# Kernel tuning notes

Hardware: AMD Instinct MI355X
Metric: run time of the kernel (lower is better)

The kernel has to match this reference:

```python
import jax, jax.numpy as jnp
import numpy as np

N, E, F_IN, D, H, G, T = 30000, 480000, 128, 32, 4, 128, 10
HD = H * D
NEG_SLOPE = 0.2


def _lin(key, fan_out, fan_in, scale=0.05):
    k1, k2 = jax.random.split(key)
    return (jax.random.normal(k1, (fan_out, fan_in), jnp.float32) * scale,
            jax.random.normal(k2, (fan_out,), jnp.float32) * scale)


def setup_inputs() -> dict:
    key = jax.random.key(0)
    ks = jax.random.split(key, 24)
    x = jax.random.normal(ks[0], (N, F_IN), jnp.float32)
    edge_index = jax.random.randint(ks[1], (2, E), 0, N, jnp.int64)
    batch = jnp.sort(jax.random.randint(ks[2], (N,), 0, G, jnp.int64))
    inp = {"x": x, "edge_index": edge_index, "batch": batch}
    # conv 0 (in=F_IN) and conv 1 (in=D); each followed by Linear(HD -> D)
    for i, fin in enumerate([F_IN, D]):
        base = 3 + i * 8
        Wl, bl = _lin(ks[base + 0], HD, fin)
        Wr, br = _lin(ks[base + 1], HD, fin)
        att = jax.random.normal(ks[base + 2], (H, D), jnp.float32) * 0.05
        bias = jnp.zeros((HD,), jnp.float32)
        lw, lb = _lin(ks[base + 3], D, HD)
        inp.update({f"Wl{i}": Wl, f"bl{i}": bl, f"Wr{i}": Wr, f"br{i}": br,
                    f"att{i}": att, f"cb{i}": bias, f"lw{i}": lw, f"lb{i}": lb})
    inp["fc1_W"], inp["fc1_b"] = _lin(ks[20], D, D)
    inp["fc2_W"], inp["fc2_b"] = _lin(ks[21], T, D)
    return inp


def _gatv2_conv(x, src, dst, Wl, bl, Wr, br, att, bias):
    # PyG GATv2Conv, concat=True, add_self_loops already applied to src/dst,
    # aggr='mean', eval mode (no dropout).
    n = x.shape[0]
    xl = (x @ Wl.T + bl).reshape(n, H, D)
    xr = (x @ Wr.T + br).reshape(n, H, D)
    e = jax.nn.leaky_relu(xl[src] + xr[dst], NEG_SLOPE)          # [E', H, D]
    alpha = jnp.einsum('ehd,hd->eh', e, att)                      # [E', H]
    amax = jax.ops.segment_max(alpha, dst, num_segments=n)        # [n, H]
    ex = jnp.exp(alpha - amax[dst])
    denom = jax.ops.segment_sum(ex, dst, num_segments=n)
    a = ex / denom[dst]                                           # softmax per target
    msg = xl[src] * a[:, :, None]                                 # [E', H, D]
    s = jax.ops.segment_sum(msg, dst, num_segments=n)
    cnt = jax.ops.segment_sum(jnp.ones((src.shape[0],), jnp.float32), dst, num_segments=n)
    out = s / cnt[:, None, None]                                  # mean aggregation
    return out.reshape(n, HD) + bias


def reference(x, edge_index, batch,
              Wl0, bl0, Wr0, br0, att0, cb0, lw0, lb0,
              Wl1, bl1, Wr1, br1, att1, cb1, lw1, lb1,
              fc1_W, fc1_b, fc2_W, fc2_b):
    loop = jnp.arange(N, dtype=edge_index.dtype)
    src = jnp.concatenate([edge_index[0], loop])  # add self loops
    dst = jnp.concatenate([edge_index[1], loop])
    convs = [(Wl0, bl0, Wr0, br0, att0, cb0, lw0, lb0),
             (Wl1, bl1, Wr1, br1, att1, cb1, lw1, lb1)]
    h = x
    for (Wl, bl, Wr, br, att, cb, lw, lb) in convs:
        h = _gatv2_conv(h, src, dst, Wl, bl, Wr, br, att, cb)
        h = h @ lw.T + lb  # heads>1: Linear(H*D -> D)
    g = jax.ops.segment_max(h, batch, num_segments=G)  # global max pool
    g = jax.nn.relu(g @ fc1_W.T + fc1_b)
    return g @ fc2_W.T + fc2_b
```

## Files before the change

### kernel.cpp

```cpp
#include <hip/hip_runtime.h>
#include <hip/hip_bf16.h>

#define NEG_SLOPE 0.2f
#define GGRP 128
#define TOUT 10

__global__ void init_kernel(int* __restrict__ deg, float* __restrict__ gpool,
                            int n, int gsize) {
    int i = blockIdx.x * blockDim.x + threadIdx.x;
    if (i < n) deg[i] = 0;
    if (i < gsize) gpool[i] = -__builtin_inff();
}

__global__ void degree_kernel(const int* __restrict__ dst, int* __restrict__ deg, int E) {
    int i = blockIdx.x * blockDim.x + threadIdx.x;
    int base = i * 4;
    if (base + 3 < E) {
        int4 d = *(const int4*)(dst + base);
        atomicAdd(&deg[d.x], 1); atomicAdd(&deg[d.y], 1);
        atomicAdd(&deg[d.z], 1); atomicAdd(&deg[d.w], 1);
    } else {
        for (int k = base; k < E; ++k) atomicAdd(&deg[dst[k]], 1);
    }
}

__global__ __launch_bounds__(256)
void scanA_kernel(const int* __restrict__ deg, int* __restrict__ rowptr,
                  int* __restrict__ bsum, int n) {
    __shared__ int wsum[4];
    int tid = threadIdx.x, lane = tid & 63, wid = tid >> 6;
    int idx = blockIdx.x * 256 + tid;
    int v = (idx < n) ? deg[idx] : 0;
    int x = v;
    #pragma unroll
    for (int off = 1; off < 64; off <<= 1) {
        int t = __shfl_up(x, off, 64);
        if (lane >= off) x += t;
    }
    if (lane == 63) wsum[wid] = x;
    __syncthreads();
    if (tid == 0) {
        int s = 0;
        #pragma unroll
        for (int i = 0; i < 4; ++i) { int t = wsum[i]; wsum[i] = s; s += t; }
        bsum[blockIdx.x] = s;
    }
    __syncthreads();
    int excl = x - v + wsum[wid];
    if (idx < n) rowptr[idx] = excl;
}

__global__ void scanB_kernel(const int* __restrict__ bsum, int* __restrict__ boff,
                             int* __restrict__ rowptr, int n, int nb) {
    int lane = threadIdx.x;
    int v0 = (lane < nb) ? bsum[lane] : 0;
    int v1 = (64 + lane < nb) ? bsum[64 + lane] : 0;
    int s0 = v0, s1 = v1;
    #pragma unroll
    for (int off = 1; off < 64; off <<= 1) {
        int t0 = __shfl_up(s0, off, 64);
        int t1 = __shfl_up(s1, off, 64);
        if (lane >= off) { s0 += t0; s1 += t1; }
    }
    int tot0 = __shfl(s0, 63, 64);
    s1 += tot0;
    boff[lane] = s0 - v0;
    boff[64 + lane] = s1 - v1;
    if (lane == 63) rowptr[n] = s1;
}

__global__ void scanC_kernel(int* __restrict__ rowptr, int* __restrict__ cursor,
                             const int* __restrict__ boff, int n) {
    int idx = blockIdx.x * blockDim.x + threadIdx.x;
    if (idx < n) {
        int r = rowptr[idx] + boff[idx >> 8];
        rowptr[idx] = r;
        cursor[idx] = r;
    }
}

__global__ void scatter_kernel(const int* __restrict__ src, const int* __restrict__ dst,
                               int* __restrict__ cursor, int* __restrict__ csr, int E) {
    int i = blockIdx.x * blockDim.x + threadIdx.x;
    int base = i * 4;
    if (base + 3 < E) {
        int4 s = *(const int4*)(src + base);
        int4 d = *(const int4*)(dst + base);
        csr[atomicAdd(&cursor[d.x], 1)] = s.x;
        csr[atomicAdd(&cursor[d.y], 1)] = s.y;
        csr[atomicAdd(&cursor[d.z], 1)] = s.z;
        csr[atomicAdd(&cursor[d.w], 1)] = s.w;
    } else {
        for (int k = base; k < E; ++k)
            csr[atomicAdd(&cursor[dst[k]], 1)] = src[k];
    }
}

template <int FIN>
__global__ __launch_bounds__(256, 2)
void gemm_tile_kernel(const float* __restrict__ X,
                      const float* __restrict__ Wl, const float* __restrict__ bl,
                      const float* __restrict__ Wr, const float* __restrict__ br,
                      float* __restrict__ xl, float* __restrict__ xr,
                      int n, int nRowBlk) {
    constexpr int BK = 32, BM = 128, LDA = BM + 4;
    constexpr int NCHUNK = FIN / BK;
    __shared__ float Xs[BK][LDA];
    __shared__ float Ws[BK][LDA];
    int tid = threadIdx.x;
    int rowBlk = blockIdx.x;
    int colBlk = 0;
    if (rowBlk >= nRowBlk) { rowBlk -= nRowBlk; colBlk = 1; }
    const float* __restrict__ Wb = colBlk ? Wr : Wl;
    const float* __restrict__ bb = colBlk ? br : bl;
    float* __restrict__ ob = colBlk ? xr : xl;
    int row0 = rowBlk * BM;

    int sr  = tid >> 3;
    int skq = (tid & 7) * 4;

    float4 xpre[4], wpre[4];

    auto load_pre = [&](int c) {
        int k0 = c * BK;
        #pragma unroll
        for (int i = 0; i < 4; ++i) {
            int r = sr + i * 32;
            int gr = row0 + r;
            float4 v = {0.f, 0.f, 0.f, 0.f};
            if (gr < n) v = *(const float4*)&X[(size_t)gr * FIN + k0 + skq];
            xpre[i] = v;
            wpre[i] = *(const float4*)&Wb[(size_t)r * FIN + k0 + skq];
        }
    };
    auto store_pre = [&]() {
        #pragma unroll
        for (int i = 0; i < 4; ++i) {
            int r = sr + i * 32;
            Xs[skq + 0][r] = xpre[i].x; Xs[skq + 1][r] = xpre[i].y;
            Xs[skq + 2][r] = xpre[i].z; Xs[skq + 3][r] = xpre[i].w;
            Ws[skq + 0][r] = wpre[i].x; Ws[skq + 1][r] = wpre[i].y;
            Ws[skq + 2][r] = wpre[i].z; Ws[skq + 3][r] = wpre[i].w;
        }
    };

    load_pre(0);
    store_pre();
    __syncthreads();

    int tx = tid & 15;
    int ty = tid >> 4;
    float acc[8][8];
    #pragma unroll
    for (int i = 0; i < 8; ++i)
        #pragma unroll
        for (int j = 0; j < 8; ++j) acc[i][j] = 0.f;

    #pragma unroll
    for (int c = 0; c < NCHUNK; ++c) {
        if (c + 1 < NCHUNK) load_pre(c + 1);
        #pragma unroll 8
        for (int k = 0; k < BK; ++k) {
            float4 a0 = *(const float4*)&Xs[k][ty * 8];
            float4 a1 = *(const float4*)&Xs[k][ty * 8 + 4];
            float4 b0 = *(const float4*)&Ws[k][tx * 8];
            float4 b1 = *(const float4*)&Ws[k][tx * 8 + 4];
            float av[8] = {a0.x, a0.y, a0.z, a0.w, a1.x, a1.y, a1.z, a1.w};
            float bv[8] = {b0.x, b0.y, b0.z, b0.w, b1.x, b1.y, b1.z, b1.w};
            #pragma unroll
            for (int i = 0; i < 8; ++i)
                #pragma unroll
                for (int j = 0; j < 8; ++j)
                    acc[i][j] = fmaf(av[i], bv[j], acc[i][j]);
        }
        if (c + 1 < NCHUNK) {
            __syncthreads();
            store_pre();
            __syncthreads();
        }
    }

    float bias[8];
    #pragma unroll
    for (int j = 0; j < 8; ++j) bias[j] = bb[tx * 8 + j];
    #pragma unroll
    for (int i = 0; i < 8; ++i) {
        int gr = row0 + ty * 8 + i;
        if (gr < n) {
            float4 o0, o1;
            o0.x = acc[i][0] + bias[0]; o0.y = acc[i][1] + bias[1];
            o0.z = acc[i][2] + bias[2]; o0.w = acc[i][3] + bias[3];
            o1.x = acc[i][4] + bias[4]; o1.y = acc[i][5] + bias[5];
            o1.z = acc[i][6] + bias[6]; o1.w = acc[i][7] + bias[7];
            *(float4*)&ob[(size_t)gr * 128 + tx * 8]     = o0;
            *(float4*)&ob[(size_t)gr * 128 + tx * 8 + 4] = o1;
        }
    }
}

__global__ __launch_bounds__(256)
void gat_fused_kernel(const float* __restrict__ xl, const float* __restrict__ xr,
                      const float* __restrict__ att, const float* __restrict__ cb,
                      const float* __restrict__ lw, const float* __restrict__ lb,
                      const int* __restrict__ rowptr, const int* __restrict__ csr,
                      float* __restrict__ out , int n) {
    __shared__ float lws[32][132];
    __shared__ float oslot[4][128];
    int tid = threadIdx.x;
    #pragma unroll
    for (int i = 0; i < 16; ++i) {
        int idx = tid + i * 256;
        lws[idx >> 7][idx & 127] = lw[idx];
    }
    __syncthreads();

    int wid = tid >> 6, lane = tid & 63;
    int q4  = lane >> 4;
    int l16 = lane & 15;
    int f8  = l16 * 8;
    int half = lane >> 5;
    int l32  = lane & 31;

    const float4 atA = *(const float4*)(att + f8);
    const float4 atB = *(const float4*)(att + f8 + 4);
    const float4 cbA = *(const float4*)(cb + f8);
    const float4 cbB = *(const float4*)(cb + f8 + 4);
    float lbv = lb[l32];

    int ndBase = blockIdx.x * 16 + wid * 4;

    for (int j = 0; j < 4; ++j) {
        int nd = ndBase + j;
        if (nd >= n) break;

        const float4 xrA  = *(const float4*)(xr + (size_t)nd * 128 + f8);
        const float4 xrB  = *(const float4*)(xr + (size_t)nd * 128 + f8 + 4);
        const float4 xlsA = *(const float4*)(xl + (size_t)nd * 128 + f8);
        const float4 xlsB = *(const float4*)(xl + (size_t)nd * 128 + f8 + 4);

        int start = rowptr[nd], end = rowptr[nd + 1];

        float den;
        float accA[4] = {0.f, 0.f, 0.f, 0.f};
        float accB[4] = {0.f, 0.f, 0.f, 0.f};

        {
            float e0 = xlsA.x + xrA.x; e0 = e0 > 0.f ? e0 : NEG_SLOPE * e0;
            float e1 = xlsA.y + xrA.y; e1 = e1 > 0.f ? e1 : NEG_SLOPE * e1;
            float e2 = xlsA.z + xrA.z; e2 = e2 > 0.f ? e2 : NEG_SLOPE * e2;
            float e3 = xlsA.w + xrA.w; e3 = e3 > 0.f ? e3 : NEG_SLOPE * e3;
            float e4 = xlsB.x + xrB.x; e4 = e4 > 0.f ? e4 : NEG_SLOPE * e4;
            float e5 = xlsB.y + xrB.y; e5 = e5 > 0.f ? e5 : NEG_SLOPE * e5;
            float e6 = xlsB.z + xrB.z; e6 = e6 > 0.f ? e6 : NEG_SLOPE * e6;
            float e7 = xlsB.w + xrB.w; e7 = e7 > 0.f ? e7 : NEG_SLOPE * e7;
            float q = e0 * atA.x + e1 * atA.y + e2 * atA.z + e3 * atA.w
                    + e4 * atB.x + e5 * atB.y + e6 * atB.z + e7 * atB.w;
            q += __shfl_xor(q, 1); q += __shfl_xor(q, 2);
            float a = __expf(q);
            if (q4 == 0) {
                den = a;
                accA[0] = a * xlsA.x; accA[1] = a * xlsA.y;
                accA[2] = a * xlsA.z; accA[3] = a * xlsA.w;
                accB[0] = a * xlsB.x; accB[1] = a * xlsB.y;
                accB[2] = a * xlsB.z; accB[3] = a * xlsB.w;
            } else {
                den = 0.f;
            }
        }

        int i = start + q4;
        int sA = (i < end) ? csr[i] : 0;
        int sB = (i + 4 < end) ? csr[i + 4] : 0;
        float4 pre0 = {0.f, 0.f, 0.f, 0.f}, pre1 = pre0;
        if (i < end) {
            pre0 = *(const float4*)(xl + (size_t)sA * 128 + f8);
            pre1 = *(const float4*)(xl + (size_t)sA * 128 + f8 + 4);
        }
        for (; i < end; i += 4) {
            float4 x0 = pre0, x1 = pre1;
            sA = sB;
            if (i + 8 < end) sB = csr[i + 8];
            if (i + 4 < end) {
                pre0 = *(const float4*)(xl + (size_t)sA * 128 + f8);
                pre1 = *(const float4*)(xl + (size_t)sA * 128 + f8 + 4);
            }
            float e0 = x0.x + xrA.x; e0 = e0 > 0.f ? e0 : NEG_SLOPE * e0;
            float e1 = x0.y + xrA.y; e1 = e1 > 0.f ? e1 : NEG_SLOPE * e1;
            float e2 = x0.z + xrA.z; e2 = e2 > 0.f ? e2 : NEG_SLOPE * e2;
            float e3 = x0.w + xrA.w; e3 = e3 > 0.f ? e3 : NEG_SLOPE * e3;
            float e4 = x1.x + xrB.x; e4 = e4 > 0.f ? e4 : NEG_SLOPE * e4;
            float e5 = x1.y + xrB.y; e5 = e5 > 0.f ? e5 : NEG_SLOPE * e5;
            float e6 = x1.z + xrB.z; e6 = e6 > 0.f ? e6 : NEG_SLOPE * e6;
            float e7 = x1.w + xrB.w; e7 = e7 > 0.f ? e7 : NEG_SLOPE * e7;
            float q = e0 * atA.x + e1 * atA.y + e2 * atA.z + e3 * atA.w
                    + e4 * atB.x + e5 * atB.y + e6 * atB.z + e7 * atB.w;
            q += __shfl_xor(q, 1); q += __shfl_xor(q, 2);
            float a = __expf(q);
            den += a;
            accA[0] = fmaf(a, x0.x, accA[0]); accA[1] = fmaf(a, x0.y, accA[1]);
            accA[2] = fmaf(a, x0.z, accA[2]); accA[3] = fmaf(a, x0.w, accA[3]);
            accB[0] = fmaf(a, x1.x, accB[0]); accB[1] = fmaf(a, x1.y, accB[1]);
            accB[2] = fmaf(a, x1.z, accB[2]); accB[3] = fmaf(a, x1.w, accB[3]);
        }

        #pragma unroll
        for (int t = 0; t < 4; ++t) {
            accA[t] += __shfl_xor(accA[t], 16); accA[t] += __shfl_xor(accA[t], 32);
            accB[t] += __shfl_xor(accB[t], 16); accB[t] += __shfl_xor(accB[t], 32);
        }
        den += __shfl_xor(den, 16); den += __shfl_xor(den, 32);

        float inv = 1.0f / (den * (float)(end - start + 1));
        if (q4 == 0) {
            float4 oA, oB;
            oA.x = fmaf(accA[0], inv, cbA.x); oA.y = fmaf(accA[1], inv, cbA.y);
            oA.z = fmaf(accA[2], inv, cbA.z); oA.w = fmaf(accA[3], inv, cbA.w);
            oB.x = fmaf(accB[0], inv, cbB.x); oB.y = fmaf(accB[1], inv, cbB.y);
            oB.z = fmaf(accB[2], inv, cbB.z); oB.w = fmaf(accB[3], inv, cbB.w);
            *(float4*)&oslot[wid][f8]     = oA;
            *(float4*)&oslot[wid][f8 + 4] = oB;
        }
        asm volatile("s_waitcnt lgkmcnt(0)" ::: "memory");

        float y = 0.f;
        int kbase = half * 64;
        #pragma unroll
        for (int k = 0; k < 64; k += 4) {
            float4 lv = *(const float4*)&lws[l32][kbase + k];
            float4 ov = *(const float4*)&oslot[wid][kbase + k];
            y = fmaf(lv.x, ov.x, y);
            y = fmaf(lv.y, ov.y, y);
            y = fmaf(lv.z, ov.z, y);
            y = fmaf(lv.w, ov.w, y);
        }
        y += __shfl_xor(y, 32);
        if (half == 0) out[(size_t)nd * 32 + l32] = y + lbv;
    }
}

__device__ __forceinline__ void atomicMaxFloat(float* addr, float val) {
    if (val >= 0.f) atomicMax((int*)addr, __float_as_int(val));
    else atomicMin((unsigned int*)addr, (unsigned int)__float_as_int(val));
}

__global__ void pool_kernel(const float* __restrict__ H, const int* __restrict__ batch,
                            float* __restrict__ g, int n) {
    int tid = threadIdx.x;
    int dim = tid & 31;
    int sub = tid >> 5;
    int nodeStart = blockIdx.x * 128 + sub * 16;
    float m = -__builtin_inff();
    int cur = -1;
    for (int j = 0; j < 16; ++j) {
        int nd = nodeStart + j;
        if (nd >= n) break;
        int b = batch[nd];
        if (b != cur) {
            if (cur >= 0) atomicMaxFloat(&g[cur * 32 + dim], m);
            cur = b; m = -__builtin_inff();
        }
        m = fmaxf(m, H[nd * 32 + dim]);
    }
    if (cur >= 0) atomicMaxFloat(&g[cur * 32 + dim], m);
}

__global__ __launch_bounds__(256)
void fc_kernel(const float* __restrict__ g,
               const float* __restrict__ fc1W, const float* __restrict__ fc1b,
               const float* __restrict__ fc2W, const float* __restrict__ fc2b,
               float* __restrict__ out) {
    __shared__ float g1[GGRP * 32];
    int tid = threadIdx.x;
    for (int idx = tid; idx < GGRP * 32; idx += 256) {
        int r = idx >> 5, c = idx & 31;
        float acc = fc1b[c];
        #pragma unroll
        for (int k = 0; k < 32; ++k) acc = fmaf(g[r * 32 + k], fc1W[c * 32 + k], acc);
        g1[idx] = acc > 0.f ? acc : 0.f;
    }
    __syncthreads();
    for (int idx = tid; idx < GGRP * TOUT; idx += 256) {
        int r = idx / TOUT, c = idx - r * TOUT;
        float acc = fc2b[c];
        #pragma unroll
        for (int k = 0; k < 32; ++k) acc = fmaf(g1[r * 32 + k], fc2W[c * 32 + k], acc);
        out[idx] = acc;
    }
}

extern "C" void kernel_launch(void* const* d_in, const int* in_sizes, int n_in,
                              void* d_out, int out_size, void* d_ws, size_t ws_size,
                              hipStream_t stream) {
    const float* x     = (const float*)d_in[0];
    const int*   ei    = (const int*)d_in[1];
    const int*   batch = (const int*)d_in[2];
    const float* Wl0 = (const float*)d_in[3];
    const float* bl0 = (const float*)d_in[4];
    const float* Wr0 = (const float*)d_in[5];
    const float* br0 = (const float*)d_in[6];
    const float* at0 = (const float*)d_in[7];
    const float* cb0 = (const float*)d_in[8];
    const float* lw0 = (const float*)d_in[9];
    const float* lb0 = (const float*)d_in[10];
    const float* Wl1 = (const float*)d_in[11];
    const float* bl1 = (const float*)d_in[12];
    const float* Wr1 = (const float*)d_in[13];
    const float* br1 = (const float*)d_in[14];
    const float* at1 = (const float*)d_in[15];
    const float* cb1 = (const float*)d_in[16];
    const float* lw1 = (const float*)d_in[17];
    const float* lb1 = (const float*)d_in[18];
    const float* fc1W = (const float*)d_in[19];
    const float* fc1b = (const float*)d_in[20];
    const float* fc2W = (const float*)d_in[21];
    const float* fc2b = (const float*)d_in[22];

    const int n = in_sizes[0] / 128;
    const int E = in_sizes[1] / 2;
    const int* src = ei;
    const int* dst = ei + E;
    const int nblkScan = (n + 255) / 256;
    const int nRowBlk = (n + 127) / 128;
    const int E4 = (E + 3) / 4;

    size_t off = 0;
    auto alloc = [&](size_t bytes) {
        void* p = (char*)d_ws + off;
        off += (bytes + 255) & ~(size_t)255;
        return p;
    };
    float* xl    = (float*)alloc((size_t)n * 128 * 4);
    float* xr    = (float*)alloc((size_t)n * 128 * 4);
    float* hbuf  = (float*)alloc((size_t)n * 32 * 4);
    int* deg     = (int*)alloc((size_t)n * 4);
    int* rowptr  = (int*)alloc((size_t)(n + 1) * 4);
    int* cursor  = (int*)alloc((size_t)n * 4);
    int* csr     = (int*)alloc((size_t)E * 4);
    int* bsum    = (int*)alloc(128 * 4);
    int* boff    = (int*)alloc(128 * 4);
    float* gpool = (float*)alloc((size_t)GGRP * 32 * 4);

    init_kernel<<<(n + 255) / 256, 256, 0, stream>>>(deg, gpool, n, GGRP * 32);
    degree_kernel<<<(E4 + 255) / 256, 256, 0, stream>>>(dst, deg, E);
    scanA_kernel<<<nblkScan, 256, 0, stream>>>(deg, rowptr, bsum, n);
    scanB_kernel<<<1, 64, 0, stream>>>(bsum, boff, rowptr, n, nblkScan);
    scanC_kernel<<<nblkScan, 256, 0, stream>>>(rowptr, cursor, boff, n);
    scatter_kernel<<<(E4 + 255) / 256, 256, 0, stream>>>(src, dst, cursor, csr, E);

    gemm_tile_kernel<128><<<2 * nRowBlk, 256, 0, stream>>>(x, Wl0, bl0, Wr0, br0,
                                                           xl, xr, n, nRowBlk);
    gat_fused_kernel<<<(n + 15) / 16, 256, 0, stream>>>(xl, xr, at0, cb0, lw0, lb0,
                                                        rowptr, csr, hbuf, n);
    gemm_tile_kernel<32><<<2 * nRowBlk, 256, 0, stream>>>(hbuf, Wl1, bl1, Wr1, br1,
                                                          xl, xr, n, nRowBlk);
    gat_fused_kernel<<<(n + 15) / 16, 256, 0, stream>>>(xl, xr, at1, cb1, lw1, lb1,
                                                        rowptr, csr, hbuf, n);

    pool_kernel<<<(n + 127) / 128, 256, 0, stream>>>(hbuf, batch, gpool, n);
    fc_kernel<<<1, 256, 0, stream>>>(gpool, fc1W, fc1b, fc2W, fc2b, (float*)d_out);
}
```

Measured before the change: 315.0 us.

## Store byte offsets in CSR, drop gather bounds checks, one node per wave

The scatter now stores source indices pre-shifted into byte offsets, and the CSR gets a zero-padded tail, so the GAT gather loop can prefetch without bounds checks or index multiplies. The GAT kernel maps one destination node per wavefront (4 per block) instead of looping over 4 nodes per wave, giving more blocks and parallelism at the cost of reloading lw into shared memory 4x more often. The separate scanB kernel is folded into scanC, where each block reduces the block sums itself, which removes one launch. Using 32-bit byte offsets limits the node count to about 4M.

New measurement: 308.0 us. -2.2%, faster.

```diff
diff --git a/kernel.cpp b/kernel.cpp
--- a/kernel.cpp
+++ b/kernel.cpp
@@ -6,10 +6,11 @@
 #define TOUT 10
 
 __global__ void init_kernel(int* __restrict__ deg, float* __restrict__ gpool,
-                            int n, int gsize) {
+                            int* __restrict__ csr_pad, int n, int gsize) {
     int i = blockIdx.x * blockDim.x + threadIdx.x;
     if (i < n) deg[i] = 0;
     if (i < gsize) gpool[i] = -__builtin_inff();
+    if (i < 64) csr_pad[i] = 0;
 }
 
 __global__ void degree_kernel(const int* __restrict__ dst, int* __restrict__ deg, int E) {
@@ -50,30 +51,33 @@
     if (idx < n) rowptr[idx] = excl;
 }
 
-__global__ void scanB_kernel(const int* __restrict__ bsum, int* __restrict__ boff,
-                             int* __restrict__ rowptr, int n, int nb) {
-    int lane = threadIdx.x;
-    int v0 = (lane < nb) ? bsum[lane] : 0;
-    int v1 = (64 + lane < nb) ? bsum[64 + lane] : 0;
-    int s0 = v0, s1 = v1;
-    #pragma unroll
-    for (int off = 1; off < 64; off <<= 1) {
-        int t0 = __shfl_up(s0, off, 64);
-        int t1 = __shfl_up(s1, off, 64);
-        if (lane >= off) { s0 += t0; s1 += t1; }
-    }
-    int tot0 = __shfl(s0, 63, 64);
-    s1 += tot0;
-    boff[lane] = s0 - v0;
-    boff[64 + lane] = s1 - v1;
-    if (lane == 63) rowptr[n] = s1;
-}
-
-__global__ void scanC_kernel(int* __restrict__ rowptr, int* __restrict__ cursor,
-                             const int* __restrict__ boff, int n) {
-    int idx = blockIdx.x * blockDim.x + threadIdx.x;
+__global__ __launch_bounds__(256)
+void scanC_kernel(int* __restrict__ rowptr, int* __restrict__ cursor,
+                  const int* __restrict__ bsum, int n, int nb) {
+    __shared__ int soff_sh;
+    int tid = threadIdx.x;
+    int bx = blockIdx.x;
+    if (tid < 64) {
+        int lane = tid;
+        int v = 0;
+        if (lane < nb && lane < bx) v = bsum[lane];
+        if (lane + 64 < nb && lane + 64 < bx) v += bsum[lane + 64];
+        #pragma unroll
+        for (int off = 32; off >= 1; off >>= 1) v += __shfl_xor(v, off, 64);
+        if (lane == 0) soff_sh = v;
+        if (bx == 0) {
+            int t = 0;
+            if (lane < nb) t = bsum[lane];
+            if (lane + 64 < nb) t += bsum[lane + 64];
+            #pragma unroll
+            for (int off = 32; off >= 1; off >>= 1) t += __shfl_xor(t, off, 64);
+            if (lane == 0) rowptr[n] = t;
+        }
+    }
+    __syncthreads();
+    int idx = bx * 256 + tid;
     if (idx < n) {
-        int r = rowptr[idx] + boff[idx >> 8];
+        int r = rowptr[idx] + soff_sh;
         rowptr[idx] = r;
         cursor[idx] = r;
     }
@@ -86,13 +90,13 @@
     if (base + 3 < E) {
         int4 s = *(const int4*)(src + base);
         int4 d = *(const int4*)(dst + base);
-        csr[atomicAdd(&cursor[d.x], 1)] = s.x;
-        csr[atomicAdd(&cursor[d.y], 1)] = s.y;
-        csr[atomicAdd(&cursor[d.z], 1)] = s.z;
-        csr[atomicAdd(&cursor[d.w], 1)] = s.w;
+        csr[atomicAdd(&cursor[d.x], 1)] = s.x << 9;
+        csr[atomicAdd(&cursor[d.y], 1)] = s.y << 9;
+        csr[atomicAdd(&cursor[d.z], 1)] = s.z << 9;
+        csr[atomicAdd(&cursor[d.w], 1)] = s.w << 9;
     } else {
         for (int k = base; k < E; ++k)
-            csr[atomicAdd(&cursor[dst[k]], 1)] = src[k];
+            csr[atomicAdd(&cursor[dst[k]], 1)] = src[k] << 9;
     }
 }
 
@@ -202,7 +206,7 @@
 void gat_fused_kernel(const float* __restrict__ xl, const float* __restrict__ xr,
                       const float* __restrict__ att, const float* __restrict__ cb,
                       const float* __restrict__ lw, const float* __restrict__ lb,
-                      const int* __restrict__ rowptr, const int* __restrict__ csr,
+                      const int* __restrict__ rowptr, const int* __restrict__ csrb,
                       float* __restrict__ out , int n) {
     __shared__ float lws[32][132];
     __shared__ float oslot[4][128];
@@ -215,127 +219,121 @@
     __syncthreads();
 
     int wid = tid >> 6, lane = tid & 63;
+    int nd = blockIdx.x * 4 + wid;
+    if (nd >= n) return;
     int q4  = lane >> 4;
     int l16 = lane & 15;
-    int f8  = l16 * 8;
+    int fb  = l16 * 32;
+
+    const char* __restrict__ xlb = (const char*)xl;
+    const char* __restrict__ xrb = (const char*)xr;
+    int selfoff = nd << 9;
+
+    const float4 xrA  = *(const float4*)(xrb + selfoff + fb);
+    const float4 xrB  = *(const float4*)(xrb + selfoff + fb + 16);
+    const float4 atA  = *(const float4*)((const char*)att + fb);
+    const float4 atB  = *(const float4*)((const char*)att + fb + 16);
+    const float4 xlsA = *(const float4*)(xlb + selfoff + fb);
+    const float4 xlsB = *(const float4*)(xlb + selfoff + fb + 16);
+
+    int start = rowptr[nd], end = rowptr[nd + 1];
+    float cnt = (float)(end - start + 1);
+
+    float den;
+    float accA[4], accB[4];
+
+    {
+        float e0 = xlsA.x + xrA.x; e0 = fmaf(NEG_SLOPE, fminf(e0, 0.f), fmaxf(e0, 0.f));
+        float e1 = xlsA.y + xrA.y; e1 = fmaf(NEG_SLOPE, fminf(e1, 0.f), fmaxf(e1, 0.f));
+        float e2 = xlsA.z + xrA.z; e2 = fmaf(NEG_SLOPE, fminf(e2, 0.f), fmaxf(e2, 0.f));
+        float e3 = xlsA.w + xrA.w; e3 = fmaf(NEG_SLOPE, fminf(e3, 0.f), fmaxf(e3, 0.f));
+        float e4 = xlsB.x + xrB.x; e4 = fmaf(NEG_SLOPE, fminf(e4, 0.f), fmaxf(e4, 0.f));
+        float e5 = xlsB.y + xrB.y; e5 = fmaf(NEG_SLOPE, fminf(e5, 0.f), fmaxf(e5, 0.f));
+        float e6 = xlsB.z + xrB.z; e6 = fmaf(NEG_SLOPE, fminf(e6, 0.f), fmaxf(e6, 0.f));
+        float e7 = xlsB.w + xrB.w; e7 = fmaf(NEG_SLOPE, fminf(e7, 0.f), fmaxf(e7, 0.f));
+        float q = e0 * atA.x + e1 * atA.y + e2 * atA.z + e3 * atA.w
+                + e4 * atB.x + e5 * atB.y + e6 * atB.z + e7 * atB.w;
+        q += __shfl_xor(q, 1); q += __shfl_xor(q, 2);
+        float a = __expf(q);
+        if (q4 == 0) {
+            den = a;
+            accA[0] = a * xlsA.x; accA[1] = a * xlsA.y;
+            accA[2] = a * xlsA.z; accA[3] = a * xlsA.w;
+            accB[0] = a * xlsB.x; accB[1] = a * xlsB.y;
+            accB[2] = a * xlsB.z; accB[3] = a * xlsB.w;
+        } else {
+            den = 0.f;
+            accA[0] = accA[1] = accA[2] = accA[3] = 0.f;
+            accB[0] = accB[1] = accB[2] = accB[3] = 0.f;
+        }
+    }
+
+    int i = start + q4;
+    int offA = csrb[i];
+    int offB = csrb[i + 4];
+    float4 pre0 = *(const float4*)(xlb + offA + fb);
+    float4 pre1 = *(const float4*)(xlb + offA + fb + 16);
+    for (; i < end; i += 4) {
+        float4 x0 = pre0, x1 = pre1;
+        offA = offB;
+        offB = csrb[i + 8];
+        pre0 = *(const float4*)(xlb + offA + fb);
+        pre1 = *(const float4*)(xlb + offA + fb + 16);
+        float e0 = x0.x + xrA.x; e0 = fmaf(NEG_SLOPE, fminf(e0, 0.f), fmaxf(e0, 0.f));
+        float e1 = x0.y + xrA.y; e1 = fmaf(NEG_SLOPE, fminf(e1, 0.f), fmaxf(e1, 0.f));
+        float e2 = x0.z + xrA.z; e2 = fmaf(NEG_SLOPE, fminf(e2, 0.f), fmaxf(e2, 0.f));
+        float e3 = x0.w + xrA.w; e3 = fmaf(NEG_SLOPE, fminf(e3, 0.f), fmaxf(e3, 0.f));
+        float e4 = x1.x + xrB.x; e4 = fmaf(NEG_SLOPE, fminf(e4, 0.f), fmaxf(e4, 0.f));
+        float e5 = x1.y + xrB.y; e5 = fmaf(NEG_SLOPE, fminf(e5, 0.f), fmaxf(e5, 0.f));
+        float e6 = x1.z + xrB.z; e6 = fmaf(NEG_SLOPE, fminf(e6, 0.f), fmaxf(e6, 0.f));
+        float e7 = x1.w + xrB.w; e7 = fmaf(NEG_SLOPE, fminf(e7, 0.f), fmaxf(e7, 0.f));
+        float q = e0 * atA.x + e1 * atA.y + e2 * atA.z + e3 * atA.w
+                + e4 * atB.x + e5 * atB.y + e6 * atB.z + e7 * atB.w;
+        q += __shfl_xor(q, 1); q += __shfl_xor(q, 2);
+        float a = __expf(q);
+        den += a;
+        accA[0] = fmaf(a, x0.x, accA[0]); accA[1] = fmaf(a, x0.y, accA[1]);
+        accA[2] = fmaf(a, x0.z, accA[2]); accA[3] = fmaf(a, x0.w, accA[3]);
+        accB[0] = fmaf(a, x1.x, accB[0]); accB[1] = fmaf(a, x1.y, accB[1]);
+        accB[2] = fmaf(a, x1.z, accB[2]); accB[3] = fmaf(a, x1.w, accB[3]);
+    }
+
+    #pragma unroll
+    for (int t = 0; t < 4; ++t) {
+        accA[t] += __shfl_xor(accA[t], 16); accA[t] += __shfl_xor(accA[t], 32);
+        accB[t] += __shfl_xor(accB[t], 16); accB[t] += __shfl_xor(accB[t], 32);
+    }
+    den += __shfl_xor(den, 16); den += __shfl_xor(den, 32);
+
+    float inv = 1.0f / (den * cnt);
+    if (q4 == 0) {
+        const float4 cbA = *(const float4*)((const char*)cb + fb);
+        const float4 cbB = *(const float4*)((const char*)cb + fb + 16);
+        float4 oA, oB;
+        oA.x = fmaf(accA[0], inv, cbA.x); oA.y = fmaf(accA[1], inv, cbA.y);
+        oA.z = fmaf(accA[2], inv, cbA.z); oA.w = fmaf(accA[3], inv, cbA.w);
+        oB.x = fmaf(accB[0], inv, cbB.x); oB.y = fmaf(accB[1], inv, cbB.y);
+        oB.z = fmaf(accB[2], inv, cbB.z); oB.w = fmaf(accB[3], inv, cbB.w);
+        *(float4*)((char*)&oslot[wid][0] + fb)      = oA;
+        *(float4*)((char*)&oslot[wid][0] + fb + 16) = oB;
+    }
+    asm volatile("s_waitcnt lgkmcnt(0)" ::: "memory");
+
     int half = lane >> 5;
-    int l32  = lane & 31;
-
-    const float4 atA = *(const float4*)(att + f8);
-    const float4 atB = *(const float4*)(att + f8 + 4);
-    const float4 cbA = *(const float4*)(cb + f8);
-    const float4 cbB = *(const float4*)(cb + f8 + 4);
-    float lbv = lb[l32];
-
-    int ndBase = blockIdx.x * 16 + wid * 4;
-
-    for (int j = 0; j < 4; ++j) {
-        int nd = ndBase + j;
-        if (nd >= n) break;
-
-        const float4 xrA  = *(const float4*)(xr + (size_t)nd * 128 + f8);
-        const float4 xrB  = *(const float4*)(xr + (size_t)nd * 128 + f8 + 4);
-        const float4 xlsA = *(const float4*)(xl + (size_t)nd * 128 + f8);
-        const float4 xlsB = *(const float4*)(xl + (size_t)nd * 128 + f8 + 4);
-
-        int start = rowptr[nd], end = rowptr[nd + 1];
-
-        float den;
-        float accA[4] = {0.f, 0.f, 0.f, 0.f};
-        float accB[4] = {0.f, 0.f, 0.f, 0.f};
-
-        {
-            float e0 = xlsA.x + xrA.x; e0 = e0 > 0.f ? e0 : NEG_SLOPE * e0;
-            float e1 = xlsA.y + xrA.y; e1 = e1 > 0.f ? e1 : NEG_SLOPE * e1;
-            float e2 = xlsA.z + xrA.z; e2 = e2 > 0.f ? e2 : NEG_SLOPE * e2;
-            float e3 = xlsA.w + xrA.w; e3 = e3 > 0.f ? e3 : NEG_SLOPE * e3;
-            float e4 = xlsB.x + xrB.x; e4 = e4 > 0.f ? e4 : NEG_SLOPE * e4;
-            float e5 = xlsB.y + xrB.y; e5 = e5 > 0.f ? e5 : NEG_SLOPE * e5;
-            float e6 = xlsB.z + xrB.z; e6 = e6 > 0.f ? e6 : NEG_SLOPE * e6;
-            float e7 = xlsB.w + xrB.w; e7 = e7 > 0.f ? e7 : NEG_SLOPE * e7;
-            float q = e0 * atA.x + e1 * atA.y + e2 * atA.z + e3 * atA.w
-                    + e4 * atB.x + e5 * atB.y + e6 * atB.z + e7 * atB.w;
-            q += __shfl_xor(q, 1); q += __shfl_xor(q, 2);
-            float a = __expf(q);
-            if (q4 == 0) {
-                den = a;
-                accA[0] = a * xlsA.x; accA[1] = a * xlsA.y;
-                accA[2] = a * xlsA.z; accA[3] = a * xlsA.w;
-                accB[0] = a * xlsB.x; accB[1] = a * xlsB.y;
-                accB[2] = a * xlsB.z; accB[3] = a * xlsB.w;
-            } else {
-                den = 0.f;
-            }
-        }
-
-        int i = start + q4;
-        int sA = (i < end) ? csr[i] : 0;
-        int sB = (i + 4 < end) ? csr[i + 4] : 0;
-        float4 pre0 = {0.f, 0.f, 0.f, 0.f}, pre1 = pre0;
-        if (i < end) {
-            pre0 = *(const float4*)(xl + (size_t)sA * 128 + f8);
-            pre1 = *(const float4*)(xl + (size_t)sA * 128 + f8 + 4);
-        }
-        for (; i < end; i += 4) {
-            float4 x0 = pre0, x1 = pre1;
-            sA = sB;
-            if (i + 8 < end) sB = csr[i + 8];
-            if (i + 4 < end) {
-                pre0 = *(const float4*)(xl + (size_t)sA * 128 + f8);
-                pre1 = *(const float4*)(xl + (size_t)sA * 128 + f8 + 4);
-            }
-            float e0 = x0.x + xrA.x; e0 = e0 > 0.f ? e0 : NEG_SLOPE * e0;
-            float e1 = x0.y + xrA.y; e1 = e1 > 0.f ? e1 : NEG_SLOPE * e1;
-            float e2 = x0.z + xrA.z; e2 = e2 > 0.f ? e2 : NEG_SLOPE * e2;
-            float e3 = x0.w + xrA.w; e3 = e3 > 0.f ? e3 : NEG_SLOPE * e3;
-            float e4 = x1.x + xrB.x; e4 = e4 > 0.f ? e4 : NEG_SLOPE * e4;
-            float e5 = x1.y + xrB.y; e5 = e5 > 0.f ? e5 : NEG_SLOPE * e5;
-            float e6 = x1.z + xrB.z; e6 = e6 > 0.f ? e6 : NEG_SLOPE * e6;
-            float e7 = x1.w + xrB.w; e7 = e7 > 0.f ? e7 : NEG_SLOPE * e7;
-            float q = e0 * atA.x + e1 * atA.y + e2 * atA.z + e3 * atA.w
-                    + e4 * atB.x + e5 * atB.y + e6 * atB.z + e7 * atB.w;
-            q += __shfl_xor(q, 1); q += __shfl_xor(q, 2);
-            float a = __expf(q);
-            den += a;
-            accA[0] = fmaf(a, x0.x, accA[0]); accA[1] = fmaf(a, x0.y, accA[1]);
-            accA[2] = fmaf(a, x0.z, accA[2]); accA[3] = fmaf(a, x0.w, accA[3]);
-            accB[0] = fmaf(a, x1.x, accB[0]); accB[1] = fmaf(a, x1.y, accB[1]);
-            accB[2] = fmaf(a, x1.z, accB[2]); accB[3] = fmaf(a, x1.w, accB[3]);
-        }
-
-        #pragma unroll
-        for (int t = 0; t < 4; ++t) {
-            accA[t] += __shfl_xor(accA[t], 16); accA[t] += __shfl_xor(accA[t], 32);
-            accB[t] += __shfl_xor(accB[t], 16); accB[t] += __shfl_xor(accB[t], 32);
-        }
-        den += __shfl_xor(den, 16); den += __shfl_xor(den, 32);
-
-        float inv = 1.0f / (den * (float)(end - start + 1));
-        if (q4 == 0) {
-            float4 oA, oB;
-            oA.x = fmaf(accA[0], inv, cbA.x); oA.y = fmaf(accA[1], inv, cbA.y);
-            oA.z = fmaf(accA[2], inv, cbA.z); oA.w = fmaf(accA[3], inv, cbA.w);
-            oB.x = fmaf(accB[0], inv, cbB.x); oB.y = fmaf(accB[1], inv, cbB.y);
-            oB.z = fmaf(accB[2], inv, cbB.z); oB.w = fmaf(accB[3], inv, cbB.w);
-            *(float4*)&oslot[wid][f8]     = oA;
-            *(float4*)&oslot[wid][f8 + 4] = oB;
-        }
-        asm volatile("s_waitcnt lgkmcnt(0)" ::: "memory");
-
-        float y = 0.f;
-        int kbase = half * 64;
-        #pragma unroll
-        for (int k = 0; k < 64; k += 4) {
-            float4 lv = *(const float4*)&lws[l32][kbase + k];
-            float4 ov = *(const float4*)&oslot[wid][kbase + k];
-            y = fmaf(lv.x, ov.x, y);
-            y = fmaf(lv.y, ov.y, y);
-            y = fmaf(lv.z, ov.z, y);
-            y = fmaf(lv.w, ov.w, y);
-        }
-        y += __shfl_xor(y, 32);
-        if (half == 0) out[(size_t)nd * 32 + l32] = y + lbv;
-    }
+    int l32 = lane & 31;
+    float y = 0.f;
+    int kbase = half * 64;
+    #pragma unroll
+    for (int k = 0; k < 64; k += 4) {
+        float4 lv = *(const float4*)&lws[l32][kbase + k];
+        float4 ov = *(const float4*)&oslot[wid][kbase + k];
+        y = fmaf(lv.x, ov.x, y);
+        y = fmaf(lv.y, ov.y, y);
+        y = fmaf(lv.z, ov.z, y);
+        y = fmaf(lv.w, ov.w, y);
+    }
+    y += __shfl_xor(y, 32);
+    if (half == 0) out[(size_t)nd * 32 + l32] = y + lb[l32];
 }
 
 __device__ __forceinline__ void atomicMaxFloat(float* addr, float val) {
@@ -435,26 +433,24 @@
     int* deg     = (int*)alloc((size_t)n * 4);
     int* rowptr  = (int*)alloc((size_t)(n + 1) * 4);
     int* cursor  = (int*)alloc((size_t)n * 4);
-    int* csr     = (int*)alloc((size_t)E * 4);
+    int* csr     = (int*)alloc((size_t)(E + 64) * 4);
     int* bsum    = (int*)alloc(128 * 4);
-    int* boff    = (int*)alloc(128 * 4);
     float* gpool = (float*)alloc((size_t)GGRP * 32 * 4);
 
-    init_kernel<<<(n + 255) / 256, 256, 0, stream>>>(deg, gpool, n, GGRP * 32);
+    init_kernel<<<(n + 255) / 256, 256, 0, stream>>>(deg, gpool, csr + E, n, GGRP * 32);
     degree_kernel<<<(E4 + 255) / 256, 256, 0, stream>>>(dst, deg, E);
     scanA_kernel<<<nblkScan, 256, 0, stream>>>(deg, rowptr, bsum, n);
-    scanB_kernel<<<1, 64, 0, stream>>>(bsum, boff, rowptr, n, nblkScan);
-    scanC_kernel<<<nblkScan, 256, 0, stream>>>(rowptr, cursor, boff, n);
+    scanC_kernel<<<nblkScan, 256, 0, stream>>>(rowptr, cursor, bsum, n, nblkScan);
     scatter_kernel<<<(E4 + 255) / 256, 256, 0, stream>>>(src, dst, cursor, csr, E);
 
     gemm_tile_kernel<128><<<2 * nRowBlk, 256, 0, stream>>>(x, Wl0, bl0, Wr0, br0,
                                                            xl, xr, n, nRowBlk);
-    gat_fused_kernel<<<(n + 15) / 16, 256, 0, stream>>>(xl, xr, at0, cb0, lw0, lb0,
-                                                        rowptr, csr, hbuf, n);
+    gat_fused_kernel<<<(n + 3) / 4, 256, 0, stream>>>(xl, xr, at0, cb0, lw0, lb0,
+                                                      rowptr, csr, hbuf, n);
     gemm_tile_kernel<32><<<2 * nRowBlk, 256, 0, stream>>>(hbuf, Wl1, bl1, Wr1, br1,
                                                           xl, xr, n, nRowBlk);
-    gat_fused_kernel<<<(n + 15) / 16, 256, 0, stream>>>(xl, xr, at1, cb1, lw1, lb1,
-                                                        rowptr, csr, hbuf, n);
+    gat_fused_kernel<<<(n + 3) / 4, 256, 0, stream>>>(xl, xr, at1, cb1, lw1, lb1,
+                                                      rowptr, csr, hbuf, n);
 
     pool_kernel<<<(n + 127) / 128, 256, 0, stream>>>(hbuf, batch, gpool, n);
     fc_kernel<<<1, 256, 0, stream>>>(gpool, fc1W, fc1b, fc2W, fc2b, (float*)d_out);
```
